# Optimization experiments

Hardware: AMD Instinct MI355X
Metric: run time of the kernel (lower is better)

The kernel has to match this reference:

```python
import jax, jax.numpy as jnp
import numpy as np


def setup_inputs() -> dict:
    key = jax.random.key(0)
    k1, k2, k3, k4, k5 = jax.random.split(key, 5)
    B, S, K, N, G = 4, 2048, 4096, 4096, 64  # G = group_size -> num_groups = K // G = 64
    x = jax.random.normal(k1, (B, S, K), dtype=jnp.float32)
    # int2 codes stored one-per-int8 slot (low 2 bits valid); use int32 container
    weight_q = jax.random.randint(k2, (N, K), 0, 4, dtype=jnp.int32)
    scale = jax.random.uniform(k3, (N, K // G), dtype=jnp.float32) * 0.05 + 0.01
    zp = jax.random.uniform(k4, (N, K // G), dtype=jnp.float32) * 3.0
    bias = jax.random.normal(k5, (N,), dtype=jnp.float32)
    return {"x": x, "weight_q": weight_q, "scale": scale, "zp": zp, "bias": bias}


def _dequant(weight_q, scale, zp):
    # weight_q: [N, K] int codes in [0,4); scale/zp: [N, num_groups]
    N, K = weight_q.shape
    num_groups = scale.shape[1]
    gs = K // num_groups  # group_size
    q = weight_q.astype(jnp.float32).reshape(N, num_groups, gs)
    w = (q - zp[:, :, None]) * scale[:, :, None]
    return w.reshape(N, K)


def reference(x, weight_q, scale, zp, bias):
    # asymm_qw2_gemm: out = x @ dequant(W)^T + bias
    w = _dequant(weight_q, scale, zp)            # [N, K]
    out = jnp.einsum('bsk,nk->bsn', x, w)        # [B, S, N]
    return out + bias
```

## Files before the change

### kernel.cpp

```cpp
#include <hip/hip_runtime.h>
#include <stdint.h>


typedef __attribute__((ext_vector_type(4))) float  f32x4;
typedef __attribute__((ext_vector_type(4))) int    i32x4;
typedef __attribute__((ext_vector_type(8))) __bf16 bf16x8;
typedef __attribute__((ext_vector_type(4))) unsigned short u16x4;

__device__ __forceinline__ unsigned short f2bf(float f) {
  unsigned u = __builtin_bit_cast(unsigned, f);
  u += 0x7fffu + ((u >> 16) & 1u);
  return (unsigned short)(u >> 16);
}

__device__ __forceinline__ void async16(const void* g, void* l) {
  __builtin_amdgcn_global_load_lds(
      (const __attribute__((address_space(1))) unsigned int*)g,
      (__attribute__((address_space(3))) unsigned int*)l, 16, 0, 0);
}

__global__ __launch_bounds__(256) void prep_kernel(
    const float* __restrict__ x, unsigned short* __restrict__ xb, int xchunks,
    const int* __restrict__ wq, const float* __restrict__ scale,
    const float* __restrict__ zp, unsigned short* __restrict__ wb,
    int wchunks, int K, int G) {
  int xblocks = (xchunks + 255) >> 8;
  if ((int)blockIdx.x < xblocks) {
    int i = blockIdx.x * 256 + threadIdx.x;
    if (i >= xchunks) return;
    f32x4 a = ((const f32x4*)x)[i];
    u16x4 o;
    o[0] = f2bf(a[0]); o[1] = f2bf(a[1]); o[2] = f2bf(a[2]); o[3] = f2bf(a[3]);
    *(u16x4*)(xb + (size_t)i * 4) = o;
  } else {
    int i = (blockIdx.x - xblocks) * 256 + threadIdx.x;
    if (i >= wchunks) return;
    int k4 = i * 4;
    int n = k4 / K, kk = k4 % K;
    int ng = K / G;
    int g = kk / G;
    float s = scale[(size_t)n * ng + g];
    float b = -zp[(size_t)n * ng + g] * s;
    i32x4 qv = ((const i32x4*)wq)[i];
    u16x4 o;
    o[0] = f2bf((float)qv[0] * s + b); o[1] = f2bf((float)qv[1] * s + b);
    o[2] = f2bf((float)qv[2] * s + b); o[3] = f2bf((float)qv[3] * s + b);
    *(u16x4*)(wb + (size_t)i * 4) = o;
  }
}

#define BM 256
#define BN 256
#define TK 64
#define REG 8192

__global__ __launch_bounds__(512, 2) void gemm_bt_kernel(
    const unsigned short* __restrict__ A,
    const unsigned short* __restrict__ B,
    const float* __restrict__ bias,
    float* __restrict__ C, int M, int N, int K) {
  __shared__ unsigned short As[4 * REG];
  __shared__ unsigned short Bs[4 * REG];

  const int tid  = threadIdx.x;
  const int lane = tid & 63;
  const int wave = tid >> 6;
  const int wm = wave >> 2, wn = wave & 3;
  const int q = lane >> 4, r = lane & 15;

  int id = blockIdx.x;
  {
    int nwg = gridDim.x;
    if ((nwg & 7) == 0) id = (id & 7) * (nwg >> 3) + (id >> 3);
  }
  const int nbx = N / BN;
  const int m0 = (id / nbx) * BM;
  const int n0 = (id % nbx) * BN;

  const int srow = tid >> 2;
  const int gch  = (tid & 3) ^ ((tid >> 3) & 3);
  const unsigned short* aG = A + (size_t)(m0 + srow) * K + gch * 8;
  const unsigned short* bG = B + (size_t)(n0 + srow) * K + gch * 8;
  const size_t rb = (size_t)128 * K;

  unsigned short* aS = As + tid * 8;
  unsigned short* bS = Bs + tid * 8;

  const int qc8 = (q ^ ((r >> 1) & 3)) * 8;
  const unsigned short* aRd = As + (wm * 128 + r) * 32 + qc8;
  const unsigned short* bRd = Bs + (wn * 64  + r) * 32 + qc8;

  f32x4 acc[8][4] = {};
  const int NT = K / TK;

#define STG(S, G, par, kh, kk) { \
    unsigned short* l = (S) + ((par) * 2 + (kh)) * REG; \
    async16((G) + (kk) + (kh) * 32, l); \
    async16((G) + rb + (kk) + (kh) * 32, l + 4096); }

  STG(aS, aG, 0, 0, 0) STG(bS, bG, 0, 0, 0)
  STG(aS, aG, 0, 1, 0) STG(bS, bG, 0, 1, 0)

#pragma unroll 1
  for (int t = 0; t < NT; ++t) {
    const int par = t & 1, nxt = par ^ 1;
    const int kk1 = (t + 1) * TK;
    const bool pf = (t + 1 < NT);

    if (pf) STG(aS, aG, nxt, 0, kk1)
    if (pf) asm volatile("s_waitcnt vmcnt(6)" ::: "memory");
    else    asm volatile("s_waitcnt vmcnt(4)" ::: "memory");
    __builtin_amdgcn_s_barrier();
    asm volatile("" ::: "memory");
    {
      const unsigned short* a0 = aRd + par * 2 * REG;
      const unsigned short* b0 = bRd + par * 2 * REG;
      bf16x8 bf[4], af[4];
#pragma unroll
      for (int j = 0; j < 4; ++j) bf[j] = *(const bf16x8*)&b0[j * 512];
#pragma unroll
      for (int i = 0; i < 4; ++i) af[i] = *(const bf16x8*)&a0[i * 512];
      __builtin_amdgcn_s_setprio(1);
#pragma unroll
      for (int i = 0; i < 4; ++i)
#pragma unroll
        for (int j = 0; j < 4; ++j)
          acc[i][j] = __builtin_amdgcn_mfma_f32_16x16x32_bf16(
              af[i], bf[j], acc[i][j], 0, 0, 0);
      __builtin_amdgcn_s_setprio(0);
      if (pf) STG(bS, bG, nxt, 0, kk1)
#pragma unroll
      for (int i = 0; i < 4; ++i) af[i] = *(const bf16x8*)&a0[(4 + i) * 512];
      __builtin_amdgcn_s_setprio(1);
#pragma unroll
      for (int i = 0; i < 4; ++i)
#pragma unroll
        for (int j = 0; j < 4; ++j)
          acc[4 + i][j] = __builtin_amdgcn_mfma_f32_16x16x32_bf16(
              af[i], bf[j], acc[4 + i][j], 0, 0, 0);
      __builtin_amdgcn_s_setprio(0);
    }

    if (pf) STG(aS, aG, nxt, 1, kk1)
    if (pf) asm volatile("s_waitcnt vmcnt(6)" ::: "memory");
    else    asm volatile("s_waitcnt vmcnt(0)" ::: "memory");
    __builtin_amdgcn_s_barrier();
    asm volatile("" ::: "memory");
    {
      const unsigned short* a1 = aRd + (par * 2 + 1) * REG;
      const unsigned short* b1 = bRd + (par * 2 + 1) * REG;
      bf16x8 bf[4], af[4];
#pragma unroll
      for (int j = 0; j < 4; ++j) bf[j] = *(const bf16x8*)&b1[j * 512];
#pragma unroll
      for (int i = 0; i < 4; ++i) af[i] = *(const bf16x8*)&a1[i * 512];
      __builtin_amdgcn_s_setprio(1);
#pragma unroll
      for (int i = 0; i < 4; ++i)
#pragma unroll
        for (int j = 0; j < 4; ++j)
          acc[i][j] = __builtin_amdgcn_mfma_f32_16x16x32_bf16(
              af[i], bf[j], acc[i][j], 0, 0, 0);
      __builtin_amdgcn_s_setprio(0);
      if (pf) STG(bS, bG, nxt, 1, kk1)
#pragma unroll
      for (int i = 0; i < 4; ++i) af[i] = *(const bf16x8*)&a1[(4 + i) * 512];
      __builtin_amdgcn_s_setprio(1);
#pragma unroll
      for (int i = 0; i < 4; ++i)
#pragma unroll
        for (int j = 0; j < 4; ++j)
          acc[4 + i][j] = __builtin_amdgcn_mfma_f32_16x16x32_bf16(
              af[i], bf[j], acc[4 + i][j], 0, 0, 0);
      __builtin_amdgcn_s_setprio(0);
    }
  }

  float bv[4];
#pragma unroll
  for (int j = 0; j < 4; ++j) bv[j] = bias[n0 + wn * 64 + j * 16 + r];
#pragma unroll
  for (int i = 0; i < 8; ++i) {
    int mbase = m0 + wm * 128 + i * 16 + q * 4;
#pragma unroll
    for (int e = 0; e < 4; ++e) {
      float* crow = C + (size_t)(mbase + e) * N + n0 + wn * 64 + r;
#pragma unroll
      for (int j = 0; j < 4; ++j)
        crow[j * 16] = acc[i][j][e] + bv[j];
    }
  }
}

__global__ __launch_bounds__(256) void naive_kernel(
    const float* __restrict__ x, const int* __restrict__ wq,
    const float* __restrict__ scale, const float* __restrict__ zp,
    const float* __restrict__ bias, float* __restrict__ out,
    int M, int N, int K, int G) {
  int idx = blockIdx.x * 256 + threadIdx.x;
  if (idx >= M * N) return;
  int m = idx / N, n = idx % N;
  const float* xr = x + (size_t)m * K;
  const int* wr = wq + (size_t)n * K;
  int ng = K / G;
  float acc = 0.f;
  for (int g = 0; g < ng; ++g) {
    float s = scale[(size_t)n * ng + g];
    float b = -zp[(size_t)n * ng + g] * s;
    for (int k = 0; k < G; ++k)
      acc += xr[g * G + k] * ((float)wr[g * G + k] * s + b);
  }
  out[idx] = acc + bias[n];
}

extern "C" void kernel_launch(void* const* d_in, const int* in_sizes, int n_in,
                              void* d_out, int out_size, void* d_ws, size_t ws_size,
                              hipStream_t stream) {
  const float* x     = (const float*)d_in[0];
  const int*   wq    = (const int*)d_in[1];
  const float* scale = (const float*)d_in[2];
  const float* zp    = (const float*)d_in[3];
  const float* bias  = (const float*)d_in[4];
  float* out = (float*)d_out;

  const int N  = in_sizes[4];
  const int K  = in_sizes[1] / N;
  const int ng = in_sizes[2] / N;
  const int G  = K / ng;
  const int M  = in_sizes[0] / K;

  size_t xb_bytes = (size_t)M * K * 2;
  size_t wb_bytes = (size_t)N * K * 2;
  bool divisible = (M % BM == 0) && (N % BN == 0) && (K % TK == 0);
  if (ws_size < xb_bytes + wb_bytes || !divisible) {
    int total = M * N;
    naive_kernel<<<dim3((total + 255) / 256), dim3(256), 0, stream>>>(
        x, wq, scale, zp, bias, out, M, N, K, G);
    return;
  }

  unsigned short* xb = (unsigned short*)d_ws;
  unsigned short* wb = (unsigned short*)((char*)d_ws + xb_bytes);

  int xchunks = M * K / 4;
  int wchunks = N * K / 4;
  int xblocks = (xchunks + 255) / 256;
  int wblocks = (wchunks + 255) / 256;
  prep_kernel<<<dim3(xblocks + wblocks), dim3(256), 0, stream>>>(
      x, xb, xchunks, wq, scale, zp, wb, wchunks, K, G);

  dim3 grid((M / BM) * (N / BN));
  gemm_bt_kernel<<<grid, dim3(512), 0, stream>>>(xb, wb, bias, out, M, N, K);
}
```

Baseline: 549.0 us.

## Software-pipeline LDS fragment reads across half-tiles and widen prep kernel to grid-stride

New measurement: 558.3 us. About the same (+1.7%).

```diff
diff --git a/kernel.cpp b/kernel.cpp
--- a/kernel.cpp
+++ b/kernel.cpp
@@ -5,7 +5,7 @@
 typedef __attribute__((ext_vector_type(4))) float  f32x4;
 typedef __attribute__((ext_vector_type(4))) int    i32x4;
 typedef __attribute__((ext_vector_type(8))) __bf16 bf16x8;
-typedef __attribute__((ext_vector_type(4))) unsigned short u16x4;
+typedef __attribute__((ext_vector_type(8))) unsigned short u16x8;
 
 __device__ __forceinline__ unsigned short f2bf(float f) {
   unsigned u = __builtin_bit_cast(unsigned, f);
@@ -20,32 +20,34 @@
 }
 
 __global__ __launch_bounds__(256) void prep_kernel(
-    const float* __restrict__ x, unsigned short* __restrict__ xb, int xchunks,
+    const float* __restrict__ x, unsigned short* __restrict__ xb, int xunits,
     const int* __restrict__ wq, const float* __restrict__ scale,
     const float* __restrict__ zp, unsigned short* __restrict__ wb,
-    int wchunks, int K, int G) {
-  int xblocks = (xchunks + 255) >> 8;
-  if ((int)blockIdx.x < xblocks) {
-    int i = blockIdx.x * 256 + threadIdx.x;
-    if (i >= xchunks) return;
-    f32x4 a = ((const f32x4*)x)[i];
-    u16x4 o;
+    int wunits, int K, int G, int ng) {
+  const int stride = gridDim.x * 256;
+  const int i0 = blockIdx.x * 256 + threadIdx.x;
+  for (int u = i0; u < xunits; u += stride) {
+    const f32x4* xp = (const f32x4*)x + (size_t)u * 2;
+    f32x4 a = xp[0], b = xp[1];
+    u16x8 o;
     o[0] = f2bf(a[0]); o[1] = f2bf(a[1]); o[2] = f2bf(a[2]); o[3] = f2bf(a[3]);
-    *(u16x4*)(xb + (size_t)i * 4) = o;
-  } else {
-    int i = (blockIdx.x - xblocks) * 256 + threadIdx.x;
-    if (i >= wchunks) return;
-    int k4 = i * 4;
-    int n = k4 / K, kk = k4 % K;
-    int ng = K / G;
+    o[4] = f2bf(b[0]); o[5] = f2bf(b[1]); o[6] = f2bf(b[2]); o[7] = f2bf(b[3]);
+    *((u16x8*)xb + u) = o;
+  }
+  for (int u = i0; u < wunits; u += stride) {
+    int k8 = u * 8;
+    int n = k8 / K, kk = k8 % K;
     int g = kk / G;
-    float s = scale[(size_t)n * ng + g];
-    float b = -zp[(size_t)n * ng + g] * s;
-    i32x4 qv = ((const i32x4*)wq)[i];
-    u16x4 o;
-    o[0] = f2bf((float)qv[0] * s + b); o[1] = f2bf((float)qv[1] * s + b);
-    o[2] = f2bf((float)qv[2] * s + b); o[3] = f2bf((float)qv[3] * s + b);
-    *(u16x4*)(wb + (size_t)i * 4) = o;
+    float s  = scale[(size_t)n * ng + g];
+    float bz = -zp[(size_t)n * ng + g] * s;
+    const i32x4* wp = (const i32x4*)wq + (size_t)u * 2;
+    i32x4 qa = wp[0], qb = wp[1];
+    u16x8 o;
+    o[0] = f2bf((float)qa[0] * s + bz); o[1] = f2bf((float)qa[1] * s + bz);
+    o[2] = f2bf((float)qa[2] * s + bz); o[3] = f2bf((float)qa[3] * s + bz);
+    o[4] = f2bf((float)qb[0] * s + bz); o[5] = f2bf((float)qb[1] * s + bz);
+    o[6] = f2bf((float)qb[2] * s + bz); o[7] = f2bf((float)qb[3] * s + bz);
+    *((u16x8*)wb + u) = o;
   }
 }
 
@@ -98,81 +100,71 @@
     async16((G) + (kk) + (kh) * 32, l); \
     async16((G) + rb + (kk) + (kh) * 32, l + 4096); }
 
+#define RD4(DST, PTR, O) \
+    _Pragma("unroll") \
+    for (int i_ = 0; i_ < 4; ++i_) \
+      (DST)[i_] = *(const bf16x8*)&(PTR)[((O) + i_) * 512];
+
+#define MF16(AF, BF, RO) \
+    __builtin_amdgcn_s_setprio(1); \
+    _Pragma("unroll") \
+    for (int i_ = 0; i_ < 4; ++i_) \
+      _Pragma("unroll") \
+      for (int j_ = 0; j_ < 4; ++j_) \
+        acc[(RO) + i_][j_] = __builtin_amdgcn_mfma_f32_16x16x32_bf16( \
+            (AF)[i_], (BF)[j_], acc[(RO) + i_][j_], 0, 0, 0); \
+    __builtin_amdgcn_s_setprio(0);
+
+  bf16x8 afA[4], afB[4], bfP[4], bfQ[4];
+
   STG(aS, aG, 0, 0, 0) STG(bS, bG, 0, 0, 0)
   STG(aS, aG, 0, 1, 0) STG(bS, bG, 0, 1, 0)
+  if (NT > 1) { STG(aS, aG, 1, 0, TK) STG(bS, bG, 1, 0, TK) }
+  if (NT > 1) asm volatile("s_waitcnt vmcnt(4)" ::: "memory");
+  else        asm volatile("s_waitcnt vmcnt(0)" ::: "memory");
+  __builtin_amdgcn_s_barrier();
+  RD4(afA, aRd, 0)
+  RD4(bfP, bRd, 0)
 
 #pragma unroll 1
   for (int t = 0; t < NT; ++t) {
     const int par = t & 1, nxt = par ^ 1;
+    const bool pf = (t + 1 < NT);
     const int kk1 = (t + 1) * TK;
-    const bool pf = (t + 1 < NT);
-
-    if (pf) STG(aS, aG, nxt, 0, kk1)
-    if (pf) asm volatile("s_waitcnt vmcnt(6)" ::: "memory");
-    else    asm volatile("s_waitcnt vmcnt(4)" ::: "memory");
+    const unsigned short* a0 = aRd + (par * 2 + 0) * REG;
+    const unsigned short* a1 = aRd + (par * 2 + 1) * REG;
+    const unsigned short* b1 = bRd + (par * 2 + 1) * REG;
+
+    RD4(afB, a0, 4)
+    MF16(afA, bfP, 0)
+
+    if (pf) { STG(aS, aG, nxt, 1, kk1) STG(bS, bG, nxt, 1, kk1) }
+    RD4(afA, a1, 0)
+    RD4(bfQ, b1, 0)
+    MF16(afB, bfP, 4)
+
+    if (pf) asm volatile("s_waitcnt vmcnt(4) lgkmcnt(0)" ::: "memory");
+    else    asm volatile("s_waitcnt vmcnt(0) lgkmcnt(0)" ::: "memory");
     __builtin_amdgcn_s_barrier();
-    asm volatile("" ::: "memory");
-    {
-      const unsigned short* a0 = aRd + par * 2 * REG;
-      const unsigned short* b0 = bRd + par * 2 * REG;
-      bf16x8 bf[4], af[4];
-#pragma unroll
-      for (int j = 0; j < 4; ++j) bf[j] = *(const bf16x8*)&b0[j * 512];
-#pragma unroll
-      for (int i = 0; i < 4; ++i) af[i] = *(const bf16x8*)&a0[i * 512];
-      __builtin_amdgcn_s_setprio(1);
-#pragma unroll
-      for (int i = 0; i < 4; ++i)
-#pragma unroll
-        for (int j = 0; j < 4; ++j)
-          acc[i][j] = __builtin_amdgcn_mfma_f32_16x16x32_bf16(
-              af[i], bf[j], acc[i][j], 0, 0, 0);
-      __builtin_amdgcn_s_setprio(0);
-      if (pf) STG(bS, bG, nxt, 0, kk1)
-#pragma unroll
-      for (int i = 0; i < 4; ++i) af[i] = *(const bf16x8*)&a0[(4 + i) * 512];
-      __builtin_amdgcn_s_setprio(1);
-#pragma unroll
-      for (int i = 0; i < 4; ++i)
-#pragma unroll
-        for (int j = 0; j < 4; ++j)
-          acc[4 + i][j] = __builtin_amdgcn_mfma_f32_16x16x32_bf16(
-              af[i], bf[j], acc[4 + i][j], 0, 0, 0);
-      __builtin_amdgcn_s_setprio(0);
-    }
-
-    if (pf) STG(aS, aG, nxt, 1, kk1)
-    if (pf) asm volatile("s_waitcnt vmcnt(6)" ::: "memory");
-    else    asm volatile("s_waitcnt vmcnt(0)" ::: "memory");
-    __builtin_amdgcn_s_barrier();
-    asm volatile("" ::: "memory");
-    {
-      const unsigned short* a1 = aRd + (par * 2 + 1) * REG;
-      const unsigned short* b1 = bRd + (par * 2 + 1) * REG;
-      bf16x8 bf[4], af[4];
-#pragma unroll
-      for (int j = 0; j < 4; ++j) bf[j] = *(const bf16x8*)&b1[j * 512];
-#pragma unroll
-      for (int i = 0; i < 4; ++i) af[i] = *(const bf16x8*)&a1[i * 512];
-      __builtin_amdgcn_s_setprio(1);
-#pragma unroll
-      for (int i = 0; i < 4; ++i)
-#pragma unroll
-        for (int j = 0; j < 4; ++j)
-          acc[i][j] = __builtin_amdgcn_mfma_f32_16x16x32_bf16(
-              af[i], bf[j], acc[i][j], 0, 0, 0);
-      __builtin_amdgcn_s_setprio(0);
-      if (pf) STG(bS, bG, nxt, 1, kk1)
-#pragma unroll
-      for (int i = 0; i < 4; ++i) af[i] = *(const bf16x8*)&a1[(4 + i) * 512];
-      __builtin_amdgcn_s_setprio(1);
-#pragma unroll
-      for (int i = 0; i < 4; ++i)
-#pragma unroll
-        for (int j = 0; j < 4; ++j)
-          acc[4 + i][j] = __builtin_amdgcn_mfma_f32_16x16x32_bf16(
-              af[i], bf[j], acc[4 + i][j], 0, 0, 0);
-      __builtin_amdgcn_s_setprio(0);
+
+    RD4(afB, a1, 4)
+    MF16(afA, bfQ, 0)
+
+    if (pf) {
+      const unsigned short* na0 = aRd + (nxt * 2) * REG;
+      const unsigned short* nb0 = bRd + (nxt * 2) * REG;
+      RD4(afA, na0, 0)
+      RD4(bfP, nb0, 0)
+    }
+    if (t + 2 < NT) {
+      STG(aS, aG, par, 0, (t + 2) * TK) STG(bS, bG, par, 0, (t + 2) * TK)
+    }
+    MF16(afB, bfQ, 4)
+
+    if (pf) {
+      if (t + 2 < NT) asm volatile("s_waitcnt vmcnt(4) lgkmcnt(0)" ::: "memory");
+      else            asm volatile("s_waitcnt vmcnt(0) lgkmcnt(0)" ::: "memory");
+      __builtin_amdgcn_s_barrier();
     }
   }
 
@@ -231,7 +223,8 @@
 
   size_t xb_bytes = (size_t)M * K * 2;
   size_t wb_bytes = (size_t)N * K * 2;
-  bool divisible = (M % BM == 0) && (N % BN == 0) && (K % TK == 0);
+  bool divisible = (M % BM == 0) && (N % BN == 0) && (K % TK == 0) &&
+                   (G % 8 == 0);
   if (ws_size < xb_bytes + wb_bytes || !divisible) {
     int total = M * N;
     naive_kernel<<<dim3((total + 255) / 256), dim3(256), 0, stream>>>(
@@ -242,12 +235,10 @@
   unsigned short* xb = (unsigned short*)d_ws;
   unsigned short* wb = (unsigned short*)((char*)d_ws + xb_bytes);
 
-  int xchunks = M * K / 4;
-  int wchunks = N * K / 4;
-  int xblocks = (xchunks + 255) / 256;
-  int wblocks = (wchunks + 255) / 256;
-  prep_kernel<<<dim3(xblocks + wblocks), dim3(256), 0, stream>>>(
-      x, xb, xchunks, wq, scale, zp, wb, wchunks, K, G);
+  int xunits = M * K / 8;
+  int wunits = N * K / 8;
+  prep_kernel<<<dim3(2048), dim3(256), 0, stream>>>(
+      x, xb, xunits, wq, scale, zp, wb, wunits, K, G, ng);
 
   dim3 grid((M / BM) * (N / BN));
   gemm_bt_kernel<<<grid, dim3(512), 0, stream>>>(xb, wb, bias, out, M, N, K);
```
